# Optimization experiments

Measured on AMD Instinct MI355X. Metric: run time of the kernel, lower is better.

Reference implementation:

```python
import jax, jax.numpy as jnp
import numpy as np

B, K, D = 4, 2048, 512   # batch, time window (self._K), d_model
H, Q, V = 8, 64, 64      # heads, per-head query dim, per-head value dim


def setup_inputs() -> dict:
    key = jax.random.key(0)
    ks = jax.random.split(key, 10)
    s = 0.05
    return {
        "query": jax.random.normal(ks[0], (B, K, D), jnp.float32),
        "key":   jax.random.normal(ks[1], (B, K, D), jnp.float32),
        "value": jax.random.normal(ks[2], (B, K, D), jnp.float32),
        # stacked per-head Linear params (torch Linear: y = x W^T + b -> store as [h, D, out])
        "W_q": jax.random.normal(ks[3], (H, D, Q), jnp.float32) * s,
        "b_q": jax.random.normal(ks[4], (H, Q), jnp.float32) * s,
        "W_k": jax.random.normal(ks[5], (H, D, Q), jnp.float32) * s,
        "b_k": jax.random.normal(ks[6], (H, Q), jnp.float32) * s,
        "W_v": jax.random.normal(ks[7], (H, D, V), jnp.float32) * s,
        "b_v": jax.random.normal(ks[8], (H, V), jnp.float32) * s,
        "W_o": jax.random.normal(ks[9], (H * V, D), jnp.float32) * s,
        "b_o": jnp.zeros((D,), jnp.float32),
    }


def reference(query, key, value, W_q, b_q, W_k, b_k, W_v, b_v, W_o, b_o):
    # per-head projections, batched over heads: [B, H, K, Q/V]
    q = jnp.einsum("bkd,hdq->bhkq", query, W_q) + b_q[None, :, None, :]
    k = jnp.einsum("bkd,hdq->bhkq", key,   W_k) + b_k[None, :, None, :]
    v = jnp.einsum("bkd,hdv->bhkv", value, W_v) + b_v[None, :, None, :]
    # NOTE: original divides by sqrt(self._K) (time window), NOT sqrt(d_k)
    scores = jnp.einsum("bhkq,bhlq->bhkl", q, k) / np.sqrt(K).astype(np.float32)
    # mask == 'subsequent': causal triu mask above the diagonal
    causal = jnp.triu(jnp.ones((K, K), bool), k=1)
    scores = jnp.where(causal[None, None], -jnp.inf, scores)
    attn = jax.nn.softmax(scores, axis=-1)
    heads = jnp.einsum("bhkl,bhlv->bhkv", attn, v)          # [B, H, K, V]
    concat = heads.transpose(0, 2, 1, 3).reshape(B, K, H * V)  # concat along last dim
    return concat @ W_o + b_o
```

## Files before the change

kernel.cpp:

```cpp
#include <hip/hip_runtime.h>
#include <hip/hip_bf16.h>

typedef __attribute__((ext_vector_type(8))) short bf16x8;
typedef __attribute__((ext_vector_type(4))) float f32x4;

#define SEQ 2048
#define DM  512
#define NH  8
#define DH  64
#define QSCALE 0.031879360f

__device__ __forceinline__ unsigned short f2bf(float f) {
  unsigned int u = __float_as_uint(f);
  unsigned int r = 0x7FFFu + ((u >> 16) & 1u);
  return (unsigned short)((u + r) >> 16);
}

__device__ __forceinline__ void cvt8f(const float4& v0, const float4& v1,
                                      unsigned short* __restrict__ o) {
  o[0] = f2bf(v0.x); o[1] = f2bf(v0.y); o[2] = f2bf(v0.z); o[3] = f2bf(v0.w);
  o[4] = f2bf(v1.x); o[5] = f2bf(v1.y); o[6] = f2bf(v1.z); o[7] = f2bf(v1.w);
}

__device__ __forceinline__ void load8f(const float* __restrict__ s,
                                       unsigned short* __restrict__ o) {
  float4 v0 = *(const float4*)s;
  float4 v1 = *(const float4*)(s + 4);
  cvt8f(v0, v1, o);
}

__device__ __forceinline__ void gload16(const unsigned short* g, unsigned short* l) {
  __builtin_amdgcn_global_load_lds(
      (const __attribute__((address_space(1))) void*)g,
      (__attribute__((address_space(3))) void*)l, 16, 0, 0);
}

__global__ __launch_bounds__(256) void weight_prep(const float* __restrict__ Wq,
                                                   const float* __restrict__ Wk,
                                                   const float* __restrict__ Wv,
                                                   const float* __restrict__ Wo,
                                                   const float* __restrict__ q,
                                                   const float* __restrict__ k,
                                                   const float* __restrict__ v,
                                                   unsigned short* __restrict__ Wqt,
                                                   unsigned short* __restrict__ Wkt,
                                                   unsigned short* __restrict__ Wvt,
                                                   unsigned short* __restrict__ Wot,
                                                   unsigned short* __restrict__ Xb) {
  const int tid = threadIdx.x;
  if (blockIdx.x >= 256) {
    const int wi = blockIdx.x - 256;
    const float* src = (wi < 128) ? q : (wi < 256) ? k : v;
    const size_t off = (size_t)(wi & 127) * 32768;
    const float* s = src + off;
    unsigned short* d = Xb + (size_t)(wi >> 7) * (4u * SEQ * DM) + off;
#pragma unroll
    for (int i = 0; i < 16; ++i) {
      const size_t idx = (size_t)(tid + 256 * i) * 8;
      __align__(16) unsigned short t[8];
      load8f(s + idx, t);
      *(uint4*)(d + idx) = *(const uint4*)t;
    }
    return;
  }
  const int which = blockIdx.x >> 6, wi = blockIdx.x & 63;
  const float* src;
  unsigned short* dst;
  int R, C, r0, c0;
  if (which < 3) {
    const float* W = (which == 0) ? Wq : (which == 1) ? Wk : Wv;
    unsigned short* D = (which == 0) ? Wqt : (which == 1) ? Wkt : Wvt;
    int h = wi >> 3;
    src = W + (size_t)h * 512 * 64;
    dst = D + (size_t)h * 64 * 512;
    R = 512; C = 64; r0 = (wi & 7) * 64; c0 = 0;
  } else {
    src = Wo; dst = Wot;
    R = 512; C = 512; r0 = (wi >> 3) * 64; c0 = (wi & 7) * 64;
  }
  __shared__ __align__(16) unsigned short T[64][72];
#pragma unroll
  for (int i = 0; i < 2; ++i) {
    int c = tid + 256 * i;
    int lr = c >> 3, lc = (c & 7) * 8;
    __align__(16) unsigned short tmp[8];
    load8f(src + (size_t)(r0 + lr) * C + c0 + lc, tmp);
    *(uint4*)&T[lr][lc] = *(const uint4*)tmp;
  }
  __syncthreads();
#pragma unroll
  for (int i = 0; i < 2; ++i) {
    int c = tid + 256 * i;
    int orow = c >> 3, och = (c & 7) * 8;
    __align__(16) unsigned short tmp[8];
#pragma unroll
    for (int j = 0; j < 8; ++j) tmp[j] = T[och + j][orow];
    *(uint4*)(dst + (size_t)(c0 + orow) * R + r0 + och) = *(uint4*)tmp;
  }
}

__global__ __launch_bounds__(256, 4) void proj128(const unsigned short* __restrict__ Xb,
                                                  const unsigned short* __restrict__ Wqt,
                                                  const unsigned short* __restrict__ Wkt,
                                                  const unsigned short* __restrict__ Wvt,
                                                  const float* __restrict__ bq,
                                                  const float* __restrict__ bk,
                                                  const float* __restrict__ bv,
                                                  unsigned short* __restrict__ Qp,
                                                  unsigned short* __restrict__ Kp,
                                                  unsigned short* __restrict__ Vpt) {
  const int which = blockIdx.z;
  const unsigned short* X = Xb + (size_t)which * (4u * SEQ * DM);
  const unsigned short* Wt = (which == 0) ? Wqt : (which == 1) ? Wkt : Wvt;
  const float* bias = (which == 0) ? bq : (which == 1) ? bk : bv;
  unsigned short* out = (which == 0) ? Qp : (which == 1) ? Kp : Vpt;
  const float ps = (which == 0) ? QSCALE : 1.0f;

  const int m0 = blockIdx.x * 128;
  const int n0 = blockIdx.y * 128;
  __shared__ __align__(16) unsigned short smem[18432];
  const int tid  = threadIdx.x;
  const int wave = tid >> 6, lane = tid & 63;
  const int l15  = lane & 15, quad = lane >> 4;
  const int rb = (wave >> 1) * 64, cb = (wave & 1) * 64;

  const int srow = wave * 8 + (lane >> 3);
  const int g8   = (((lane & 7) ^ (lane >> 3)) << 3);
  const unsigned short* aSrc = X  + (size_t)(m0 + srow) * DM + g8;
  const unsigned short* bSrc = Wt + (size_t)(n0 + srow) * DM + g8;
  unsigned short* aDst = smem        + wave * 512 + lane * 8;
  unsigned short* bDst = smem + 8192 + wave * 512 + lane * 8;

  f32x4 acc[4][4];
#pragma unroll
  for (int i = 0; i < 4; ++i)
#pragma unroll
    for (int f = 0; f < 4; ++f) acc[i][f] = (f32x4){0.f, 0.f, 0.f, 0.f};

  for (int k0 = 0; k0 < DM; k0 += 64) {
    __syncthreads();
#pragma unroll
    for (int i = 0; i < 4; ++i) {
      gload16(aSrc + (size_t)(i * 32) * DM + k0, aDst + i * 2048);
      gload16(bSrc + (size_t)(i * 32) * DM + k0, bDst + i * 2048);
    }
    __syncthreads();
#pragma unroll
    for (int kc = 0; kc < 2; ++kc) {
      bf16x8 av[4], bv4[4];
#pragma unroll
      for (int i = 0; i < 4; ++i)
        av[i]  = *(const bf16x8*)(smem + (size_t)(rb + 16 * i + l15) * 64 +
                                  (((kc * 4 + quad) ^ (l15 & 7)) << 3));
#pragma unroll
      for (int f = 0; f < 4; ++f)
        bv4[f] = *(const bf16x8*)(smem + 8192 + (size_t)(cb + 16 * f + l15) * 64 +
                                  (((kc * 4 + quad) ^ (l15 & 7)) << 3));
#pragma unroll
      for (int i = 0; i < 4; ++i)
#pragma unroll
        for (int f = 0; f < 4; ++f)
          acc[i][f] = __builtin_amdgcn_mfma_f32_16x16x32_bf16(av[i], bv4[f], acc[i][f], 0, 0, 0);
    }
  }

  if (which < 2) {
#pragma unroll
    for (int i = 0; i < 4; ++i)
#pragma unroll
      for (int f = 0; f < 4; ++f)
#pragma unroll
        for (int r = 0; r < 4; ++r) {
          int m = m0 + rb + 16 * i + quad * 4 + r;
          int col = n0 + cb + 16 * f + l15;
          int head = col >> 6, o = col & 63;
          int b = m >> 11, s = m & (SEQ - 1);
          float val = (acc[i][f][r] + bias[col]) * ps;
          out[(((size_t)(b * NH + head) * SEQ + s) << 6) + o] = f2bf(val);
        }
  } else {
    __syncthreads();
    unsigned short* T = smem + wave * 4608;
#pragma unroll
    for (int i = 0; i < 4; ++i)
#pragma unroll
      for (int f = 0; f < 4; ++f)
#pragma unroll
        for (int r = 0; r < 4; ++r) {
          int lrow = 16 * i + quad * 4 + r;
          int lcol = 16 * f + l15;
          int col = n0 + cb + 16 * f + l15;
          T[lcol * 72 + lrow] = f2bf(acc[i][f][r] + bias[col]);
        }
    const int mbase = m0 + rb;
    const int b = mbase >> 11, sbase = mbase & (SEQ - 1);
    const int head = (n0 + cb) >> 6;
    unsigned short* dstb = out + ((size_t)(b * NH + head) * DH) * SEQ + sbase;
#pragma unroll
    for (int j = 0; j < 8; ++j) {
      int dh = (lane >> 3) + j * 8;
      int sc = (lane & 7) * 8;
      *(uint4*)(dstb + (size_t)dh * SEQ + sc) = *(const uint4*)&T[dh * 72 + sc];
    }
  }
}

__global__ __launch_bounds__(512, 4) void attn_kernel(const unsigned short* __restrict__ Qp,
                                                      const unsigned short* __restrict__ Kp,
                                                      const unsigned short* __restrict__ Vpt,
                                                      unsigned short* __restrict__ concat) {
  const int bh = blockIdx.x;
  const int ip = blockIdx.y;
  const int b = bh >> 3, h = bh & 7;
  const int qa = ip, qb = 31 - ip;
  __shared__ __align__(16) unsigned short Ks[2][64][72], Vts[2][64][72];
  const int tid  = threadIdx.x;
  const int wave = tid >> 6, lane = tid & 63;
  const int l15  = lane & 15, quad = lane >> 4;
  const int w4   = wave & 3;
  const bool isB = wave < 4;
  const int qt   = isB ? qb : qa;
  const unsigned short* Qb = Qp  + (size_t)bh * SEQ * DH;
  const unsigned short* Kb = Kp  + (size_t)bh * SEQ * DH;
  const unsigned short* Vb = Vpt + (size_t)bh * DH * SEQ;

  bf16x8 aq[2];
#pragma unroll
  for (int kc = 0; kc < 2; ++kc)
    aq[kc] = *(const bf16x8*)(Qb + (size_t)(qt * 64 + 16 * w4 + l15) * DH + kc * 32 + quad * 8);

  float l_acc = 0.f;
  f32x4 Of[4];
#pragma unroll
  for (int f = 0; f < 4; ++f) Of[f] = (f32x4){0.f, 0.f, 0.f, 0.f};

  const int sr = tid >> 3, sc = (tid & 7) * 8;
  uint4 kst, vst;

#define STAGE_LOAD(lt_) do {                                                   \
    kst = *(const uint4*)(Kb + (size_t)((lt_) * 64 + sr) * DH + sc);           \
    vst = *(const uint4*)(Vb + (size_t)sr * SEQ + (lt_) * 64 + sc);            \
  } while (0)

#define STAGE_WRITE(bi_) do {                                                  \
    *(uint4*)&Ks[bi_][sr][sc]  = kst;                                          \
    *(uint4*)&Vts[bi_][sr][sc] = vst;                                          \
  } while (0)

#define CVTPK(d_, lo_, hi_) asm("v_cvt_pk_bf16_f32 %0, %1, %2" : "=v"(d_) : "v"(lo_), "v"(hi_))
#define PL32SWAP(a_, b_) asm("v_permlane32_swap_b32 %0, %1" : "+v"(a_), "+v"(b_))
#define PL16SWAP(a_, b_) asm("v_permlane16_swap_b32 %0, %1" : "+v"(a_), "+v"(b_))

  STAGE_LOAD(0);
  STAGE_WRITE(0);
  STAGE_LOAD(1);
  __syncthreads();

#pragma unroll 1
  for (int lt = 0; lt <= qb; ++lt) {
    const int cur = lt & 1;
    if (lt < qb) STAGE_WRITE(cur ^ 1);
    if (lt + 2 <= qb) STAGE_LOAD(lt + 2);

    const bool act = isB || (lt <= qa);
    if (act) {
      f32x4 S[4];
#pragma unroll
      for (int f = 0; f < 4; ++f) S[f] = (f32x4){0.f, 0.f, 0.f, 0.f};
#pragma unroll
      for (int kc = 0; kc < 2; ++kc) {
#pragma unroll
        for (int f = 0; f < 4; ++f) {
          bf16x8 bk = *(const bf16x8*)&Ks[cur][16 * f + l15][kc * 32 + quad * 8];
          S[f] = __builtin_amdgcn_mfma_f32_16x16x32_bf16(bk, aq[kc], S[f], 0, 0, 0);
        }
      }
      if (lt == qt) {
        const int qloc = 16 * w4 + l15;
#pragma unroll
        for (int f = 0; f < 4; ++f)
#pragma unroll
          for (int r = 0; r < 4; ++r)
            if (16 * f + 4 * quad + r > qloc) S[f][r] = -1e30f;
      }
      unsigned int P0[4], P1[4];
#pragma unroll
      for (int f = 0; f < 4; ++f) {
        float p0 = __builtin_amdgcn_exp2f(S[f][0]);
        float p1 = __builtin_amdgcn_exp2f(S[f][1]);
        float p2 = __builtin_amdgcn_exp2f(S[f][2]);
        float p3 = __builtin_amdgcn_exp2f(S[f][3]);
        l_acc += (p0 + p1) + (p2 + p3);
        CVTPK(P0[f], p0, p1);
        CVTPK(P1[f], p2, p3);
      }
#pragma unroll
      for (int kc = 0; kc < 2; ++kc) {
        unsigned int x0 = P0[2 * kc], y0 = P0[2 * kc + 1];
        unsigned int x1 = P1[2 * kc], y1 = P1[2 * kc + 1];
        PL32SWAP(x0, y0); PL16SWAP(x0, y0);
        PL32SWAP(x1, y1); PL16SWAP(x1, y1);
        union { unsigned int u[4]; bf16x8 v; } ap;
        ap.u[0] = x0; ap.u[1] = x1; ap.u[2] = y0; ap.u[3] = y1;
#pragma unroll
        for (int f = 0; f < 4; ++f) {
          bf16x8 bvv = *(const bf16x8*)&Vts[cur][16 * f + l15][kc * 32 + quad * 8];
          Of[f] = __builtin_amdgcn_mfma_f32_16x16x32_bf16(ap.v, bvv, Of[f], 0, 0, 0);
        }
      }
    }
    __syncthreads();
  }
#undef STAGE_LOAD
#undef STAGE_WRITE
#undef CVTPK
#undef PL32SWAP
#undef PL16SWAP

  l_acc += __shfl_xor(l_acc, 16);
  l_acc += __shfl_xor(l_acc, 32);
  float rl[4];
#pragma unroll
  for (int r = 0; r < 4; ++r) rl[r] = 1.0f / __shfl(l_acc, quad * 4 + r);

#pragma unroll
  for (int f = 0; f < 4; ++f)
#pragma unroll
    for (int r = 0; r < 4; ++r) {
      const int row = qt * 64 + 16 * w4 + quad * 4 + r;
      const int col = h * DH + 16 * f + l15;
      concat[(size_t)(b * SEQ + row) * DM + col] = f2bf(Of[f][r] * rl[r]);
    }
}

__global__ __launch_bounds__(256, 2) void gemm_out(const unsigned short* __restrict__ A,
                                                   const unsigned short* __restrict__ Bt,
                                                   const float* __restrict__ bias,
                                                   float* __restrict__ out) {
  const int m0 = blockIdx.x * 64;
  const int nbase = blockIdx.y * 128;
  __shared__ __align__(16) unsigned short Bs[2][64][64];
  const int tid  = threadIdx.x;
  const int wave = tid >> 6, lane = tid & 63;
  const int l15  = lane & 15, quad = lane >> 4;

  bf16x8 afr[16];
  const unsigned short* arow = A + (size_t)(m0 + 16 * wave + l15) * DM;
#pragma unroll
  for (int k0i = 0; k0i < 8; ++k0i)
#pragma unroll
    for (int kc = 0; kc < 2; ++kc)
      afr[k0i * 2 + kc] = *(const bf16x8*)(arow + k0i * 64 + kc * 32 + quad * 8);

  const int srow = wave * 8 + (lane >> 3);
  const int g8   = (((lane & 7) ^ (lane >> 3)) << 3);
  unsigned short* bDst = &Bs[0][0][0] + wave * 512 + lane * 8;

#define G_STAGE(s_, bi_) do {                                                    \
    const int n0_ = nbase + ((s_) >> 3) * 64, k0_ = ((s_) & 7) * 64;             \
    _Pragma("unroll")                                                            \
    for (int i_ = 0; i_ < 2; ++i_)                                               \
      gload16(Bt + (size_t)(n0_ + i_ * 32 + srow) * DM + k0_ + g8,               \
              bDst + (bi_) * 4096 + i_ * 2048);                                  \
  } while (0)

  f32x4 acc[2][4];
#pragma unroll
  for (int nh = 0; nh < 2; ++nh)
#pragma unroll
    for (int f = 0; f < 4; ++f) acc[nh][f] = (f32x4){0.f, 0.f, 0.f, 0.f};

  G_STAGE(0, 0);
  __syncthreads();

#pragma unroll
  for (int s = 0; s < 16; ++s) {
    const int cur = s & 1;
    if (s < 15) G_STAGE(s + 1, cur ^ 1);
    const int nh = s >> 3;
#pragma unroll
    for (int kc = 0; kc < 2; ++kc)
#pragma unroll
      for (int f = 0; f < 4; ++f) {
        bf16x8 bfv = *(const bf16x8*)(&Bs[cur][0][0] + (size_t)(16 * f + l15) * 64 +
                                      (((kc * 4 + quad) ^ (l15 & 7)) << 3));
        acc[nh][f] = __builtin_amdgcn_mfma_f32_16x16x32_bf16(afr[(s & 7) * 2 + kc], bfv, acc[nh][f], 0, 0, 0);
      }
    __syncthreads();
  }
#undef G_STAGE

#pragma unroll
  for (int nh = 0; nh < 2; ++nh)
#pragma unroll
    for (int f = 0; f < 4; ++f)
#pragma unroll
      for (int r = 0; r < 4; ++r) {
        int row = 16 * wave + quad * 4 + r;
        int col = nbase + nh * 64 + 16 * f + l15;
        out[(size_t)(m0 + row) * DM + col] = acc[nh][f][r] + bias[col];
      }
}

extern "C" void kernel_launch(void* const* d_in, const int* in_sizes, int n_in,
                              void* d_out, int out_size, void* d_ws, size_t ws_size,
                              hipStream_t stream) {
  const float* query = (const float*)d_in[0];
  const float* key   = (const float*)d_in[1];
  const float* value = (const float*)d_in[2];
  const float* W_q   = (const float*)d_in[3];
  const float* b_q   = (const float*)d_in[4];
  const float* W_k   = (const float*)d_in[5];
  const float* b_k   = (const float*)d_in[6];
  const float* W_v   = (const float*)d_in[7];
  const float* b_v   = (const float*)d_in[8];
  const float* W_o   = (const float*)d_in[9];
  const float* b_o   = (const float*)d_in[10];
  float* out = (float*)d_out;

  char* ws = (char*)d_ws;
  unsigned short* Wqt    = (unsigned short*)(ws + 0);
  unsigned short* Wkt    = (unsigned short*)(ws + 524288);
  unsigned short* Wvt    = (unsigned short*)(ws + 1048576);
  unsigned short* Wot    = (unsigned short*)(ws + 1572864);
  unsigned short* Qp     = (unsigned short*)(ws + 2097152);
  unsigned short* Kp     = (unsigned short*)(ws + 10485760);
  unsigned short* Vpt    = (unsigned short*)(ws + 18874368);
  unsigned short* concat = (unsigned short*)(ws + 27262976);
  unsigned short* Xb     = (unsigned short*)(ws + 35651584);

  weight_prep<<<dim3(640), 256, 0, stream>>>(W_q, W_k, W_v, W_o, query, key, value,
                                             Wqt, Wkt, Wvt, Wot, Xb);

  proj128<<<dim3(64, 4, 3), 256, 0, stream>>>(Xb, Wqt, Wkt, Wvt,
                                              b_q, b_k, b_v, Qp, Kp, Vpt);

  attn_kernel<<<dim3(32, 16), 512, 0, stream>>>(Qp, Kp, Vpt, concat);

  gemm_out<<<dim3(128, 4), 256, 0, stream>>>(concat, Wot, b_o, out);
}
```

Measured before the change: 176.6 us.

## Process four query tiles per attention block with 32 rows per wave

```diff
diff --git a/kernel.cpp b/kernel.cpp
--- a/kernel.cpp
+++ b/kernel.cpp
@@ -205,34 +205,38 @@
   }
 }
 
-__global__ __launch_bounds__(512, 4) void attn_kernel(const unsigned short* __restrict__ Qp,
+__global__ __launch_bounds__(512, 1) void attn_kernel(const unsigned short* __restrict__ Qp,
                                                       const unsigned short* __restrict__ Kp,
                                                       const unsigned short* __restrict__ Vpt,
                                                       unsigned short* __restrict__ concat) {
   const int bh = blockIdx.x;
-  const int ip = blockIdx.y;
+  const int p  = blockIdx.y;
   const int b = bh >> 3, h = bh & 7;
-  const int qa = ip, qb = 31 - ip;
+  const int t3 = 31 - p;
   __shared__ __align__(16) unsigned short Ks[2][64][72], Vts[2][64][72];
   const int tid  = threadIdx.x;
   const int wave = tid >> 6, lane = tid & 63;
   const int l15  = lane & 15, quad = lane >> 4;
-  const int w4   = wave & 3;
-  const bool isB = wave < 4;
-  const int qt   = isB ? qb : qa;
+  const int sub  = wave & 1;
+  const int qt = (wave < 2) ? t3 : (wave < 4) ? (23 - p) : (wave < 6) ? (p + 8) : p;
   const unsigned short* Qb = Qp  + (size_t)bh * SEQ * DH;
   const unsigned short* Kb = Kp  + (size_t)bh * SEQ * DH;
   const unsigned short* Vb = Vpt + (size_t)bh * DH * SEQ;
 
-  bf16x8 aq[2];
-#pragma unroll
-  for (int kc = 0; kc < 2; ++kc)
-    aq[kc] = *(const bf16x8*)(Qb + (size_t)(qt * 64 + 16 * w4 + l15) * DH + kc * 32 + quad * 8);
-
-  float l_acc = 0.f;
-  f32x4 Of[4];
-#pragma unroll
-  for (int f = 0; f < 4; ++f) Of[f] = (f32x4){0.f, 0.f, 0.f, 0.f};
+  bf16x8 aq[2][2];
+#pragma unroll
+  for (int hb = 0; hb < 2; ++hb)
+#pragma unroll
+    for (int kc = 0; kc < 2; ++kc)
+      aq[hb][kc] = *(const bf16x8*)(Qb + (size_t)(qt * 64 + sub * 32 + hb * 16 + l15) * DH +
+                                    kc * 32 + quad * 8);
+
+  float l_acc[2] = {0.f, 0.f};
+  f32x4 Of[2][4];
+#pragma unroll
+  for (int hb = 0; hb < 2; ++hb)
+#pragma unroll
+    for (int f = 0; f < 4; ++f) Of[hb][f] = (f32x4){0.f, 0.f, 0.f, 0.f};
 
   const int sr = tid >> 3, sc = (tid & 7) * 8;
   uint4 kst, vst;
@@ -257,55 +261,66 @@
   __syncthreads();
 
 #pragma unroll 1
-  for (int lt = 0; lt <= qb; ++lt) {
+  for (int lt = 0; lt <= t3; ++lt) {
     const int cur = lt & 1;
-    if (lt < qb) STAGE_WRITE(cur ^ 1);
-    if (lt + 2 <= qb) STAGE_LOAD(lt + 2);
-
-    const bool act = isB || (lt <= qa);
-    if (act) {
-      f32x4 S[4];
-#pragma unroll
-      for (int f = 0; f < 4; ++f) S[f] = (f32x4){0.f, 0.f, 0.f, 0.f};
+    if (lt < t3) STAGE_WRITE(cur ^ 1);
+    if (lt + 2 <= t3) STAGE_LOAD(lt + 2);
+
+    if (lt <= qt) {
+      f32x4 S[2][4];
+#pragma unroll
+      for (int hb = 0; hb < 2; ++hb)
+#pragma unroll
+        for (int f = 0; f < 4; ++f) S[hb][f] = (f32x4){0.f, 0.f, 0.f, 0.f};
 #pragma unroll
       for (int kc = 0; kc < 2; ++kc) {
 #pragma unroll
         for (int f = 0; f < 4; ++f) {
           bf16x8 bk = *(const bf16x8*)&Ks[cur][16 * f + l15][kc * 32 + quad * 8];
-          S[f] = __builtin_amdgcn_mfma_f32_16x16x32_bf16(bk, aq[kc], S[f], 0, 0, 0);
+          S[0][f] = __builtin_amdgcn_mfma_f32_16x16x32_bf16(bk, aq[0][kc], S[0][f], 0, 0, 0);
+          S[1][f] = __builtin_amdgcn_mfma_f32_16x16x32_bf16(bk, aq[1][kc], S[1][f], 0, 0, 0);
         }
       }
       if (lt == qt) {
-        const int qloc = 16 * w4 + l15;
-#pragma unroll
-        for (int f = 0; f < 4; ++f)
-#pragma unroll
-          for (int r = 0; r < 4; ++r)
-            if (16 * f + 4 * quad + r > qloc) S[f][r] = -1e30f;
-      }
-      unsigned int P0[4], P1[4];
-#pragma unroll
-      for (int f = 0; f < 4; ++f) {
-        float p0 = __builtin_amdgcn_exp2f(S[f][0]);
-        float p1 = __builtin_amdgcn_exp2f(S[f][1]);
-        float p2 = __builtin_amdgcn_exp2f(S[f][2]);
-        float p3 = __builtin_amdgcn_exp2f(S[f][3]);
-        l_acc += (p0 + p1) + (p2 + p3);
-        CVTPK(P0[f], p0, p1);
-        CVTPK(P1[f], p2, p3);
-      }
+#pragma unroll
+        for (int hb = 0; hb < 2; ++hb) {
+          const int qloc = sub * 32 + hb * 16 + l15;
+#pragma unroll
+          for (int f = 0; f < 4; ++f)
+#pragma unroll
+            for (int r = 0; r < 4; ++r)
+              if (16 * f + 4 * quad + r > qloc) S[hb][f][r] = -1e30f;
+        }
+      }
+      unsigned int P0[2][4], P1[2][4];
+#pragma unroll
+      for (int hb = 0; hb < 2; ++hb)
+#pragma unroll
+        for (int f = 0; f < 4; ++f) {
+          float p0 = __builtin_amdgcn_exp2f(S[hb][f][0]);
+          float p1 = __builtin_amdgcn_exp2f(S[hb][f][1]);
+          float p2 = __builtin_amdgcn_exp2f(S[hb][f][2]);
+          float p3 = __builtin_amdgcn_exp2f(S[hb][f][3]);
+          l_acc[hb] += (p0 + p1) + (p2 + p3);
+          CVTPK(P0[hb][f], p0, p1);
+          CVTPK(P1[hb][f], p2, p3);
+        }
 #pragma unroll
       for (int kc = 0; kc < 2; ++kc) {
-        unsigned int x0 = P0[2 * kc], y0 = P0[2 * kc + 1];
-        unsigned int x1 = P1[2 * kc], y1 = P1[2 * kc + 1];
-        PL32SWAP(x0, y0); PL16SWAP(x0, y0);
-        PL32SWAP(x1, y1); PL16SWAP(x1, y1);
-        union { unsigned int u[4]; bf16x8 v; } ap;
-        ap.u[0] = x0; ap.u[1] = x1; ap.u[2] = y0; ap.u[3] = y1;
+        union { unsigned int u[4]; bf16x8 v; } ap[2];
+#pragma unroll
+        for (int hb = 0; hb < 2; ++hb) {
+          unsigned int x0 = P0[hb][2 * kc], y0 = P0[hb][2 * kc + 1];
+          unsigned int x1 = P1[hb][2 * kc], y1 = P1[hb][2 * kc + 1];
+          PL32SWAP(x0, y0); PL16SWAP(x0, y0);
+          PL32SWAP(x1, y1); PL16SWAP(x1, y1);
+          ap[hb].u[0] = x0; ap[hb].u[1] = x1; ap[hb].u[2] = y0; ap[hb].u[3] = y1;
+        }
 #pragma unroll
         for (int f = 0; f < 4; ++f) {
           bf16x8 bvv = *(const bf16x8*)&Vts[cur][16 * f + l15][kc * 32 + quad * 8];
-          Of[f] = __builtin_amdgcn_mfma_f32_16x16x32_bf16(ap.v, bvv, Of[f], 0, 0, 0);
+          Of[0][f] = __builtin_amdgcn_mfma_f32_16x16x32_bf16(ap[0].v, bvv, Of[0][f], 0, 0, 0);
+          Of[1][f] = __builtin_amdgcn_mfma_f32_16x16x32_bf16(ap[1].v, bvv, Of[1][f], 0, 0, 0);
         }
       }
     }
@@ -317,20 +332,25 @@
 #undef PL32SWAP
 #undef PL16SWAP
 
-  l_acc += __shfl_xor(l_acc, 16);
-  l_acc += __shfl_xor(l_acc, 32);
-  float rl[4];
-#pragma unroll
-  for (int r = 0; r < 4; ++r) rl[r] = 1.0f / __shfl(l_acc, quad * 4 + r);
-
-#pragma unroll
-  for (int f = 0; f < 4; ++f)
-#pragma unroll
-    for (int r = 0; r < 4; ++r) {
-      const int row = qt * 64 + 16 * w4 + quad * 4 + r;
-      const int col = h * DH + 16 * f + l15;
-      concat[(size_t)(b * SEQ + row) * DM + col] = f2bf(Of[f][r] * rl[r]);
-    }
+#pragma unroll
+  for (int hb = 0; hb < 2; ++hb) {
+    l_acc[hb] += __shfl_xor(l_acc[hb], 16);
+    l_acc[hb] += __shfl_xor(l_acc[hb], 32);
+  }
+#pragma unroll
+  for (int hb = 0; hb < 2; ++hb) {
+    float rl[4];
+#pragma unroll
+    for (int r = 0; r < 4; ++r) rl[r] = 1.0f / __shfl(l_acc[hb], quad * 4 + r);
+#pragma unroll
+    for (int f = 0; f < 4; ++f)
+#pragma unroll
+      for (int r = 0; r < 4; ++r) {
+        const int row = qt * 64 + sub * 32 + hb * 16 + quad * 4 + r;
+        const int col = h * DH + 16 * f + l15;
+        concat[(size_t)(b * SEQ + row) * DM + col] = f2bf(Of[hb][f][r] * rl[r]);
+      }
+  }
 }
 
 __global__ __launch_bounds__(256, 2) void gemm_out(const unsigned short* __restrict__ A,
@@ -435,7 +455,7 @@
   proj128<<<dim3(64, 4, 3), 256, 0, stream>>>(Xb, Wqt, Wkt, Wvt,
                                               b_q, b_k, b_v, Qp, Kp, Vpt);
 
-  attn_kernel<<<dim3(32, 16), 512, 0, stream>>>(Qp, Kp, Vpt, concat);
+  attn_kernel<<<dim3(32, 8), 512, 0, stream>>>(Qp, Kp, Vpt, concat);
 
   gemm_out<<<dim3(128, 4), 256, 0, stream>>>(concat, Wot, b_o, out);
 }
```

Result: slower. 182.9 us (+3.6%).
